# Optimization experiments

Measured on AMD Instinct MI355X. Metric: run time of the kernel, lower is better.

Reference implementation:

```python
import jax, jax.numpy as jnp
import numpy as np

B, T, D_IN, H, L4 = 64, 512, 512, 1024, 4096  # L4 = 4*H (torch LSTMCell gate dim)


def setup_inputs() -> dict:
    key = jax.random.key(0)
    ks = jax.random.split(key, 9)
    s_in = 1.0 / np.sqrt(H)  # torch LSTMCell default init scale
    return {
        "x": jax.random.normal(ks[0], (B, T, D_IN), dtype=jnp.float32),
        "Wih0": jax.random.normal(ks[1], (L4, D_IN), dtype=jnp.float32) * s_in,
        "Whh0": jax.random.normal(ks[2], (L4, H), dtype=jnp.float32) * s_in,
        "bih0": jax.random.normal(ks[3], (L4,), dtype=jnp.float32) * s_in,
        "bhh0": jax.random.normal(ks[4], (L4,), dtype=jnp.float32) * s_in,
        "Wih1": jax.random.normal(ks[5], (L4, H), dtype=jnp.float32) * s_in,
        "Whh1": jax.random.normal(ks[6], (L4, H), dtype=jnp.float32) * s_in,
        "bih1": jax.random.normal(ks[7], (L4,), dtype=jnp.float32) * s_in,
        "bhh1": jax.random.normal(ks[8], (L4,), dtype=jnp.float32) * s_in,
    }


def _lstm_cell(x, h, c, Wih, Whh, bih, bhh):
    # torch.nn.LSTMCell: gates ordered i, f, g, o
    gates = x @ Wih.T + bih + h @ Whh.T + bhh  # [B, 4H]
    i, f, g, o = jnp.split(gates, 4, axis=-1)
    i = jax.nn.sigmoid(i)
    f = jax.nn.sigmoid(f)
    g = jnp.tanh(g)
    o = jax.nn.sigmoid(o)
    c_new = f * c + i * g
    h_new = o * jnp.tanh(c_new)
    return h_new, c_new


def reference(x, Wih0, Whh0, bih0, bhh0, Wih1, Whh1, bih1, bhh1):
    b = x.shape[0]
    h0 = jnp.zeros((b, H), dtype=x.dtype)
    zeros4 = (h0, h0, h0, h0)  # (h0, c0, h1, c1)

    def step(carry, x_t):
        h0_, c0_, h1_, c1_ = carry
        h0_, c0_ = _lstm_cell(x_t, h0_, c0_, Wih0, Whh0, bih0, bhh0)
        h1_, c1_ = _lstm_cell(h0_, h1_, c1_, Wih1, Whh1, bih1, bhh1)
        return (h0_, c0_, h1_, c1_), h1_

    _, ys = jax.lax.scan(step, zeros4, jnp.swapaxes(x, 0, 1))  # ys: [T, B, H]
    return jax.nn.sigmoid(jnp.swapaxes(ys, 0, 1))  # [B, T, H]
```

## Files before the change

kernel.cpp:

```cpp
#include <hip/hip_runtime.h>
#include <hip/hip_bf16.h>

typedef __attribute__((ext_vector_type(8))) short short8;
typedef __attribute__((ext_vector_type(4))) float f32x4;
typedef __attribute__((ext_vector_type(4))) unsigned uint4v;
typedef unsigned long long u64;

#define T_STEPS 512
#define BATCH 64
#define HID 1024
#define DIN 512
#define NBLOCKS 128
#define NTHREADS 512

#define WS_GRP 0
#define WS_ROOT 2048
#define WS_H0 4096
#define WS_H1 (4096 + 262144)
#define WS_XB (1u << 20)
#define HBUF 131072

#define MFMA __builtin_amdgcn_mfma_f32_16x16x32_bf16

__device__ __forceinline__ short bf16r(float x) {
  unsigned u = __builtin_bit_cast(unsigned, x);
  u += 0x7FFFu + ((u >> 16) & 1u);
  return (short)(u >> 16);
}

__device__ __forceinline__ float sigf(float x) {
  return 1.0f / (1.0f + __expf(-x));
}
__device__ __forceinline__ float tanh_(float x) {
  return 2.0f * sigf(2.0f * x) - 1.0f;
}

__device__ __forceinline__ short8 pack8(const float* p) {
  float4 a = *(const float4*)p;
  float4 c = *(const float4*)(p + 4);
  short8 v;
  v[0] = bf16r(a.x); v[1] = bf16r(a.y); v[2] = bf16r(a.z); v[3] = bf16r(a.w);
  v[4] = bf16r(c.x); v[5] = bf16r(c.y); v[6] = bf16r(c.z); v[7] = bf16r(c.w);
  return v;
}

__device__ __forceinline__ short8 ld_frag16(const void* base, int voff) {
  __amdgpu_buffer_rsrc_t rsrc = __builtin_amdgcn_make_buffer_rsrc(
      const_cast<void*>(base), (short)0, 0xFFFFFFFFu, 0x00020000u);
  uint4v f = __builtin_amdgcn_raw_buffer_load_b128(rsrc, voff, 0, 0x11);
  return __builtin_bit_cast(short8, f);
}

__device__ __forceinline__ void wait_gen(unsigned* root, unsigned* gen_lds,
                                         unsigned s, int tid) {
  if (tid == 256) {
    const unsigned tgt = 8u * s;
    int g = 0;
    while (__hip_atomic_load(root, __ATOMIC_RELAXED, __HIP_MEMORY_SCOPE_AGENT) < tgt) {
      __builtin_amdgcn_s_sleep(2);
      if (++g > (1 << 13)) break;
    }
    __hip_atomic_store(gen_lds, s, __ATOMIC_RELEASE, __HIP_MEMORY_SCOPE_WORKGROUP);
  }
  int g = 0;
  while (__hip_atomic_load(gen_lds, __ATOMIC_ACQUIRE, __HIP_MEMORY_SCOPE_WORKGROUP) < s) {
    __builtin_amdgcn_s_sleep(1);
    if (++g > (1 << 17)) break;
  }
}

__global__ void cast_x_kernel(const float* __restrict__ x, unsigned char* __restrict__ ws) {
  unsigned char* xb = ws + WS_XB;
  int idx = blockIdx.x * blockDim.x + threadIdx.x;
  for (int c = idx; c < 64 * 512 * 64; c += 262144) {
    const int b = c >> 15;
    const int t = (c >> 6) & 511;
    const int kc = c & 63;
    const float* src = x + (((b << 9) + t) << 9) + (kc << 3);
    short8 v = pack8(src);
    const int kt = kc >> 2;
    const int ln = (b & 15) + ((kc & 3) << 4);
    unsigned char* dst = xb + (((t << 2) + (b >> 4)) * 16 + kt) * 1024 + ln * 16;
    *(short8*)dst = v;
  }
}

__global__ __launch_bounds__(NTHREADS, 1) void lstm_main(
    const float* __restrict__ Wih0, const float* __restrict__ Whh0,
    const float* __restrict__ bih0, const float* __restrict__ bhh0,
    const float* __restrict__ Wih1, const float* __restrict__ Whh1,
    const float* __restrict__ bih1, const float* __restrict__ bhh1,
    float* __restrict__ out, unsigned char* __restrict__ ws)
{
  __shared__ float red[8][4][2][64][4];
  __shared__ float red2[8][4][2][64][4];
  __shared__ unsigned gen_lds;

  const int tid = threadIdx.x;
  const int wid = tid >> 6;
  const int lane = tid & 63;
  const int blk = blockIdx.x;
  const int lane16 = lane * 16;

  unsigned* grp = (unsigned*)(ws + WS_GRP);
  unsigned* root = (unsigned*)(ws + WS_ROOT);
  unsigned char* h0b = ws + WS_H0;
  unsigned char* h1b = ws + WS_H1;
  const unsigned char* xb = ws + WS_XB;

  short8 wf[28];
  {
    const int hi8 = (lane >> 4) << 3;
#pragma unroll
    for (int nt = 0; nt < 2; ++nt) {
      const int n = nt * 16 + (lane & 15);
      const int row = ((n >> 3) << 10) + blk * 8 + (n & 7);
#pragma unroll
      for (int i = 0; i < 2; ++i)
        wf[i * 2 + nt] = pack8(Wih0 + row * DIN + (2 * wid + i) * 32 + hi8);
#pragma unroll
      for (int i = 0; i < 4; ++i) {
        const int k = (4 * wid + i) * 32 + hi8;
        wf[4 + i * 2 + nt]  = pack8(Whh0 + row * HID + k);
        wf[12 + i * 2 + nt] = pack8(Wih1 + row * HID + k);
        wf[20 + i * 2 + nt] = pack8(Whh1 + row * HID + k);
      }
    }
  }

  const int j = tid & 7;
  const int b = tid >> 3;
  const int jg = blk * 8 + j;
  const int m = b >> 4;
  const int r = b & 15;
  float bias0[4], bias1[4];
#pragma unroll
  for (int g = 0; g < 4; ++g) {
    bias0[g] = bih0[g * HID + jg] + bhh0[g * HID + jg];
    bias1[g] = bih1[g * HID + jg] + bhh1[g * HID + jg];
  }
  float c0 = 0.0f, c1 = 0.0f;
  const int hoff = ((b >> 4) * 32 + (jg >> 5)) * 1024 +
                   ((b & 15) + 16 * ((jg >> 3) & 3)) * 16 + (jg & 7) * 2;

  if (tid == 0) __hip_atomic_store(&gen_lds, 0u, __ATOMIC_RELAXED, __HIP_MEMORY_SCOPE_WORKGROUP);
  __syncthreads();

  for (int s = 0; s <= T_STEPS; ++s) {
    const int p0 = s & 1;
    const bool doL0 = (s < T_STEPS);
    const bool doL1 = (s >= 1);
    const unsigned char* h0r = h0b + (p0 ^ 1) * HBUF;
    const unsigned char* h1r = h1b + p0 * HBUF;

    f32x4 acc0[4][2];
    if (doL0) {
      const unsigned char* xs = xb + s * 65536;
#pragma unroll
      for (int mm = 0; mm < 4; ++mm) {
        acc0[mm][0] = (f32x4){0.f, 0.f, 0.f, 0.f};
        acc0[mm][1] = (f32x4){0.f, 0.f, 0.f, 0.f};
#pragma unroll
        for (int i = 0; i < 2; ++i) {
          short8 af = *(const short8*)(xs + (mm * 16 + 2 * wid + i) * 1024 + lane16);
          acc0[mm][0] = MFMA(af, wf[i * 2 + 0], acc0[mm][0], 0, 0, 0);
          acc0[mm][1] = MFMA(af, wf[i * 2 + 1], acc0[mm][1], 0, 0, 0);
        }
      }
    }

    wait_gen(root, &gen_lds, (unsigned)s, tid);

#pragma unroll
    for (int mm = 0; mm < 4; ++mm) {
      short8 f0[4], f1[4];
#pragma unroll
      for (int i = 0; i < 4; ++i)
        f0[i] = ld_frag16(h0r, (mm * 32 + 4 * wid + i) * 1024 + lane16);
      if (doL1) {
#pragma unroll
        for (int i = 0; i < 4; ++i)
          f1[i] = ld_frag16(h1r, (mm * 32 + 4 * wid + i) * 1024 + lane16);
      }

      if (doL0) {
#pragma unroll
        for (int i = 0; i < 4; ++i) {
          acc0[mm][0] = MFMA(f0[i], wf[4 + i * 2 + 0], acc0[mm][0], 0, 0, 0);
          acc0[mm][1] = MFMA(f0[i], wf[4 + i * 2 + 1], acc0[mm][1], 0, 0, 0);
        }
        *(f32x4*)(&red[wid][mm][0][lane][0]) = acc0[mm][0];
        *(f32x4*)(&red[wid][mm][1][lane][0]) = acc0[mm][1];
      }
      if (doL1) {
        f32x4 a1n0 = {0.f, 0.f, 0.f, 0.f}, a1n1 = {0.f, 0.f, 0.f, 0.f};
#pragma unroll
        for (int i = 0; i < 4; ++i) {
          a1n0 = MFMA(f0[i], wf[12 + i * 2 + 0], a1n0, 0, 0, 0);
          a1n1 = MFMA(f0[i], wf[12 + i * 2 + 1], a1n1, 0, 0, 0);
        }
#pragma unroll
        for (int i = 0; i < 4; ++i) {
          a1n0 = MFMA(f1[i], wf[20 + i * 2 + 0], a1n0, 0, 0, 0);
          a1n1 = MFMA(f1[i], wf[20 + i * 2 + 1], a1n1, 0, 0, 0);
        }
        *(f32x4*)(&red2[wid][mm][0][lane][0]) = a1n0;
        *(f32x4*)(&red2[wid][mm][1][lane][0]) = a1n1;
      }
    }
    __syncthreads();

    if (doL0) {
      float sg[4];
#pragma unroll
      for (int g = 0; g < 4; ++g) {
        const int n = g * 8 + j;
        const int nt = n >> 4;
        const int ln = ((r >> 2) << 4) | (n & 15);
        const int rg = r & 3;
        float t = bias0[g];
#pragma unroll
        for (int w2 = 0; w2 < 8; ++w2) t += red[w2][m][nt][ln][rg];
        sg[g] = t;
      }
      const float iv = sigf(sg[0]);
      const float fv = sigf(sg[1]);
      const float gv = tanh_(sg[2]);
      const float ov = sigf(sg[3]);
      c0 = fv * c0 + iv * gv;
      const float h0v = ov * tanh_(c0);
      unsigned hb = (unsigned)bf16r(h0v) & 0xFFFFu;
      unsigned nb = (unsigned)__shfl_down((int)hb, 1) & 0xFFFFu;
      if ((j & 1) == 0)
        __hip_atomic_store((unsigned*)(h0b + p0 * HBUF + hoff), hb | (nb << 16),
                           __ATOMIC_RELAXED, __HIP_MEMORY_SCOPE_AGENT);
    }
    float outv = 0.0f;
    if (doL1) {
      float sg[4];
#pragma unroll
      for (int g = 0; g < 4; ++g) {
        const int n = g * 8 + j;
        const int nt = n >> 4;
        const int ln = ((r >> 2) << 4) | (n & 15);
        const int rg = r & 3;
        float t = bias1[g];
#pragma unroll
        for (int w2 = 0; w2 < 8; ++w2) t += red2[w2][m][nt][ln][rg];
        sg[g] = t;
      }
      const float iv = sigf(sg[0]);
      const float fv = sigf(sg[1]);
      const float gv = tanh_(sg[2]);
      const float ov = sigf(sg[3]);
      c1 = fv * c1 + iv * gv;
      const float h1v = ov * tanh_(c1);
      outv = sigf(h1v);
      unsigned hb = (unsigned)bf16r(h1v) & 0xFFFFu;
      unsigned nb = (unsigned)__shfl_down((int)hb, 1) & 0xFFFFu;
      if ((j & 1) == 0)
        __hip_atomic_store((unsigned*)(h1b + (p0 ^ 1) * HBUF + hoff), hb | (nb << 16),
                           __ATOMIC_RELAXED, __HIP_MEMORY_SCOPE_AGENT);
    }

    asm volatile("s_waitcnt vmcnt(0)" ::: "memory");
    __syncthreads();

    if (doL0 && tid == 0) {
      unsigned v = __hip_atomic_fetch_add(&grp[(blk >> 4) * 32], 1u,
                                          __ATOMIC_RELAXED, __HIP_MEMORY_SCOPE_AGENT);
      if ((v & 15) == 15)
        __hip_atomic_fetch_add(root, 1u, __ATOMIC_RELAXED, __HIP_MEMORY_SCOPE_AGENT);
    }

    if (doL1)
      __builtin_nontemporal_store(outv, &out[b * (T_STEPS * HID) + (s - 1) * HID + jg]);
  }
}

extern "C" void kernel_launch(void* const* d_in, const int* in_sizes, int n_in,
                              void* d_out, int out_size, void* d_ws, size_t ws_size,
                              hipStream_t stream) {
  const float* x    = (const float*)d_in[0];
  const float* Wih0 = (const float*)d_in[1];
  const float* Whh0 = (const float*)d_in[2];
  const float* bih0 = (const float*)d_in[3];
  const float* bhh0 = (const float*)d_in[4];
  const float* Wih1 = (const float*)d_in[5];
  const float* Whh1 = (const float*)d_in[6];
  const float* bih1 = (const float*)d_in[7];
  const float* bhh1 = (const float*)d_in[8];
  unsigned char* ws = (unsigned char*)d_ws;

  (void)hipMemsetAsync(d_ws, 0, WS_XB, stream);
  hipLaunchKernelGGL(cast_x_kernel, dim3(1024), dim3(256), 0, stream, x, ws);
  hipLaunchKernelGGL(lstm_main, dim3(NBLOCKS), dim3(NTHREADS), 0, stream,
                     Wih0, Whh0, bih0, bhh0, Wih1, Whh1, bih1, bhh1,
                     (float*)d_out, ws);
}
```

Measured before the change: 3.301 ms.

## Split work across blocks by batch half and 16 hidden units

Changes the per-block work split from all 64 batch rows by 8 hidden units to 32 batch rows (mg) by 16 hidden units (ng). Each block keeps twice as many weight fragments in registers (56 short8 instead of 28) but reads only half of the h0/h1 state fragments from global memory each step. The intent is to halve the per-step global reads of recurrent state on the latency-bound critical path and to give each A fragment more MFMAs. The cost is much higher register pressure, which could cause spills.

```diff
diff --git a/kernel.cpp b/kernel.cpp
--- a/kernel.cpp
+++ b/kernel.cpp
@@ -92,14 +92,16 @@
     const float* __restrict__ bih1, const float* __restrict__ bhh1,
     float* __restrict__ out, unsigned char* __restrict__ ws)
 {
-  __shared__ float red[8][4][2][64][4];
-  __shared__ float red2[8][4][2][64][4];
+  __shared__ float red[8][2][4][64][4];
+  __shared__ float red2[8][2][4][64][4];
   __shared__ unsigned gen_lds;
 
   const int tid = threadIdx.x;
   const int wid = tid >> 6;
   const int lane = tid & 63;
   const int blk = blockIdx.x;
+  const int mg = blk >> 6;
+  const int ng = blk & 63;
   const int lane16 = lane * 16;
 
   unsigned* grp = (unsigned*)(ws + WS_GRP);
@@ -108,31 +110,31 @@
   unsigned char* h1b = ws + WS_H1;
   const unsigned char* xb = ws + WS_XB;
 
-  short8 wf[28];
+  short8 wf[56];
   {
     const int hi8 = (lane >> 4) << 3;
 #pragma unroll
-    for (int nt = 0; nt < 2; ++nt) {
-      const int n = nt * 16 + (lane & 15);
-      const int row = ((n >> 3) << 10) + blk * 8 + (n & 7);
-#pragma unroll
-      for (int i = 0; i < 2; ++i)
-        wf[i * 2 + nt] = pack8(Wih0 + row * DIN + (2 * wid + i) * 32 + hi8);
-#pragma unroll
-      for (int i = 0; i < 4; ++i) {
-        const int k = (4 * wid + i) * 32 + hi8;
-        wf[4 + i * 2 + nt]  = pack8(Whh0 + row * HID + k);
-        wf[12 + i * 2 + nt] = pack8(Wih1 + row * HID + k);
-        wf[20 + i * 2 + nt] = pack8(Whh1 + row * HID + k);
-      }
-    }
-  }
-
-  const int j = tid & 7;
-  const int b = tid >> 3;
-  const int jg = blk * 8 + j;
-  const int m = b >> 4;
-  const int r = b & 15;
+    for (int nt = 0; nt < 4; ++nt) {
+      const int row = (nt << 10) + ng * 16 + (lane & 15);
+#pragma unroll
+      for (int kt = 0; kt < 2; ++kt)
+        wf[kt * 4 + nt] = pack8(Wih0 + row * DIN + (2 * wid + kt) * 32 + hi8);
+#pragma unroll
+      for (int kt = 0; kt < 4; ++kt) {
+        const int k = (4 * wid + kt) * 32 + hi8;
+        wf[8 + kt * 4 + nt]  = pack8(Whh0 + row * HID + k);
+        wf[24 + kt * 4 + nt] = pack8(Wih1 + row * HID + k);
+        wf[40 + kt * 4 + nt] = pack8(Whh1 + row * HID + k);
+      }
+    }
+  }
+
+  const int j = tid & 15;
+  const int bl = tid >> 4;
+  const int b = mg * 32 + bl;
+  const int jg = ng * 16 + j;
+  const int m = bl >> 4;
+  const int r = bl & 15;
   float bias0[4], bias1[4];
 #pragma unroll
   for (int g = 0; g < 4; ++g) {
@@ -153,18 +155,20 @@
     const unsigned char* h0r = h0b + (p0 ^ 1) * HBUF;
     const unsigned char* h1r = h1b + p0 * HBUF;
 
-    f32x4 acc0[4][2];
+    f32x4 acc0[2][4];
     if (doL0) {
       const unsigned char* xs = xb + s * 65536;
 #pragma unroll
-      for (int mm = 0; mm < 4; ++mm) {
-        acc0[mm][0] = (f32x4){0.f, 0.f, 0.f, 0.f};
-        acc0[mm][1] = (f32x4){0.f, 0.f, 0.f, 0.f};
-#pragma unroll
-        for (int i = 0; i < 2; ++i) {
-          short8 af = *(const short8*)(xs + (mm * 16 + 2 * wid + i) * 1024 + lane16);
-          acc0[mm][0] = MFMA(af, wf[i * 2 + 0], acc0[mm][0], 0, 0, 0);
-          acc0[mm][1] = MFMA(af, wf[i * 2 + 1], acc0[mm][1], 0, 0, 0);
+      for (int mm = 0; mm < 2; ++mm) {
+#pragma unroll
+        for (int nt = 0; nt < 4; ++nt)
+          acc0[mm][nt] = (f32x4){0.f, 0.f, 0.f, 0.f};
+#pragma unroll
+        for (int kt = 0; kt < 2; ++kt) {
+          short8 af = *(const short8*)(xs + (((2 * mg + mm) * 16) + 2 * wid + kt) * 1024 + lane16);
+#pragma unroll
+          for (int nt = 0; nt < 4; ++nt)
+            acc0[mm][nt] = MFMA(af, wf[kt * 4 + nt], acc0[mm][nt], 0, 0, 0);
         }
       }
     }
@@ -172,40 +176,45 @@
     wait_gen(root, &gen_lds, (unsigned)s, tid);
 
 #pragma unroll
-    for (int mm = 0; mm < 4; ++mm) {
+    for (int mm = 0; mm < 2; ++mm) {
+      const int tbase = (2 * mg + mm) * 32 + 4 * wid;
       short8 f0[4], f1[4];
 #pragma unroll
       for (int i = 0; i < 4; ++i)
-        f0[i] = ld_frag16(h0r, (mm * 32 + 4 * wid + i) * 1024 + lane16);
+        f0[i] = ld_frag16(h0r, (tbase + i) * 1024 + lane16);
       if (doL1) {
 #pragma unroll
         for (int i = 0; i < 4; ++i)
-          f1[i] = ld_frag16(h1r, (mm * 32 + 4 * wid + i) * 1024 + lane16);
+          f1[i] = ld_frag16(h1r, (tbase + i) * 1024 + lane16);
       }
 
       if (doL0) {
 #pragma unroll
-        for (int i = 0; i < 4; ++i) {
-          acc0[mm][0] = MFMA(f0[i], wf[4 + i * 2 + 0], acc0[mm][0], 0, 0, 0);
-          acc0[mm][1] = MFMA(f0[i], wf[4 + i * 2 + 1], acc0[mm][1], 0, 0, 0);
-        }
-        *(f32x4*)(&red[wid][mm][0][lane][0]) = acc0[mm][0];
-        *(f32x4*)(&red[wid][mm][1][lane][0]) = acc0[mm][1];
+        for (int i = 0; i < 4; ++i)
+#pragma unroll
+          for (int nt = 0; nt < 4; ++nt)
+            acc0[mm][nt] = MFMA(f0[i], wf[8 + i * 4 + nt], acc0[mm][nt], 0, 0, 0);
+#pragma unroll
+        for (int nt = 0; nt < 4; ++nt)
+          *(f32x4*)(&red[wid][mm][nt][lane][0]) = acc0[mm][nt];
       }
       if (doL1) {
-        f32x4 a1n0 = {0.f, 0.f, 0.f, 0.f}, a1n1 = {0.f, 0.f, 0.f, 0.f};
-#pragma unroll
-        for (int i = 0; i < 4; ++i) {
-          a1n0 = MFMA(f0[i], wf[12 + i * 2 + 0], a1n0, 0, 0, 0);
-          a1n1 = MFMA(f0[i], wf[12 + i * 2 + 1], a1n1, 0, 0, 0);
-        }
-#pragma unroll
-        for (int i = 0; i < 4; ++i) {
-          a1n0 = MFMA(f1[i], wf[20 + i * 2 + 0], a1n0, 0, 0, 0);
-          a1n1 = MFMA(f1[i], wf[20 + i * 2 + 1], a1n1, 0, 0, 0);
-        }
-        *(f32x4*)(&red2[wid][mm][0][lane][0]) = a1n0;
-        *(f32x4*)(&red2[wid][mm][1][lane][0]) = a1n1;
+        f32x4 a1[4];
+#pragma unroll
+        for (int nt = 0; nt < 4; ++nt) a1[nt] = (f32x4){0.f, 0.f, 0.f, 0.f};
+#pragma unroll
+        for (int i = 0; i < 4; ++i)
+#pragma unroll
+          for (int nt = 0; nt < 4; ++nt)
+            a1[nt] = MFMA(f0[i], wf[24 + i * 4 + nt], a1[nt], 0, 0, 0);
+#pragma unroll
+        for (int i = 0; i < 4; ++i)
+#pragma unroll
+          for (int nt = 0; nt < 4; ++nt)
+            a1[nt] = MFMA(f1[i], wf[40 + i * 4 + nt], a1[nt], 0, 0, 0);
+#pragma unroll
+        for (int nt = 0; nt < 4; ++nt)
+          *(f32x4*)(&red2[wid][mm][nt][lane][0]) = a1[nt];
       }
     }
     __syncthreads();
@@ -214,13 +223,11 @@
       float sg[4];
 #pragma unroll
       for (int g = 0; g < 4; ++g) {
-        const int n = g * 8 + j;
-        const int nt = n >> 4;
-        const int ln = ((r >> 2) << 4) | (n & 15);
+        const int ln = ((r >> 2) << 4) | j;
         const int rg = r & 3;
         float t = bias0[g];
 #pragma unroll
-        for (int w2 = 0; w2 < 8; ++w2) t += red[w2][m][nt][ln][rg];
+        for (int w2 = 0; w2 < 8; ++w2) t += red[w2][m][g][ln][rg];
         sg[g] = t;
       }
       const float iv = sigf(sg[0]);
@@ -240,13 +247,11 @@
       float sg[4];
 #pragma unroll
       for (int g = 0; g < 4; ++g) {
-        const int n = g * 8 + j;
-        const int nt = n >> 4;
-        const int ln = ((r >> 2) << 4) | (n & 15);
+        const int ln = ((r >> 2) << 4) | j;
         const int rg = r & 3;
         float t = bias1[g];
 #pragma unroll
-        for (int w2 = 0; w2 < 8; ++w2) t += red2[w2][m][nt][ln][rg];
+        for (int w2 = 0; w2 < 8; ++w2) t += red2[w2][m][g][ln][rg];
         sg[g] = t;
       }
       const float iv = sigf(sg[0]);
```

After: 7.100 ms. 2.15x slower.

## Replace hierarchical root barrier with split per-layer group counters polled in parallel

Applied to the files above, without the earlier changes.

The two-level counter tree, where group counters feed a single root counter, is replaced by two sets of eight group counters, one for layer 0 and one for layer 1. A full wavefront polls all sixteen counters at once and combines the checks with a vote. Layer 0 now signals completion right after its h0 stores, before the layer-1 epilogue, so other blocks can start the next step sooner. The cost is an extra fence and __syncthreads per step, plus more polling traffic on global atomics.

```diff
diff --git a/kernel.cpp b/kernel.cpp
--- a/kernel.cpp
+++ b/kernel.cpp
@@ -13,8 +13,8 @@
 #define NBLOCKS 128
 #define NTHREADS 512
 
-#define WS_GRP 0
-#define WS_ROOT 2048
+#define WS_GRP0 0
+#define WS_GRP1 1024
 #define WS_H0 4096
 #define WS_H1 (4096 + 262144)
 #define WS_XB (1u << 20)
@@ -51,16 +51,22 @@
   return __builtin_bit_cast(short8, f);
 }
 
-__device__ __forceinline__ void wait_gen(unsigned* root, unsigned* gen_lds,
-                                         unsigned s, int tid) {
-  if (tid == 256) {
-    const unsigned tgt = 8u * s;
+__device__ __forceinline__ void wait_gen2(unsigned* grp0, unsigned* grp1,
+                                          unsigned* gen_lds, unsigned s, int tid) {
+  if ((tid >> 6) == 4) {
+    const int l = tid & 63;
+    const unsigned t0 = 16u * s;
+    const unsigned t1 = (s >= 1) ? 16u * (s - 1) : 0u;
     int g = 0;
-    while (__hip_atomic_load(root, __ATOMIC_RELAXED, __HIP_MEMORY_SCOPE_AGENT) < tgt) {
-      __builtin_amdgcn_s_sleep(2);
-      if (++g > (1 << 13)) break;
-    }
-    __hip_atomic_store(gen_lds, s, __ATOMIC_RELEASE, __HIP_MEMORY_SCOPE_WORKGROUP);
+    for (;;) {
+      unsigned v0 = (l < 8) ? __hip_atomic_load(&grp0[l * 32], __ATOMIC_RELAXED, __HIP_MEMORY_SCOPE_AGENT) : ~0u;
+      unsigned v1 = (l < 8) ? __hip_atomic_load(&grp1[l * 32], __ATOMIC_RELAXED, __HIP_MEMORY_SCOPE_AGENT) : ~0u;
+      if (__all(v0 >= t0 && v1 >= t1)) break;
+      __builtin_amdgcn_s_sleep(1);
+      if (++g > (1 << 15)) break;
+    }
+    if (l == 0)
+      __hip_atomic_store(gen_lds, s, __ATOMIC_RELEASE, __HIP_MEMORY_SCOPE_WORKGROUP);
   }
   int g = 0;
   while (__hip_atomic_load(gen_lds, __ATOMIC_ACQUIRE, __HIP_MEMORY_SCOPE_WORKGROUP) < s) {
@@ -102,8 +108,8 @@
   const int blk = blockIdx.x;
   const int lane16 = lane * 16;
 
-  unsigned* grp = (unsigned*)(ws + WS_GRP);
-  unsigned* root = (unsigned*)(ws + WS_ROOT);
+  unsigned* grp0 = (unsigned*)(ws + WS_GRP0);
+  unsigned* grp1 = (unsigned*)(ws + WS_GRP1);
   unsigned char* h0b = ws + WS_H0;
   unsigned char* h1b = ws + WS_H1;
   const unsigned char* xb = ws + WS_XB;
@@ -169,7 +175,7 @@
       }
     }
 
-    wait_gen(root, &gen_lds, (unsigned)s, tid);
+    wait_gen2(grp0, grp1, &gen_lds, (unsigned)s, tid);
 
 #pragma unroll
     for (int mm = 0; mm < 4; ++mm) {
@@ -235,6 +241,12 @@
         __hip_atomic_store((unsigned*)(h0b + p0 * HBUF + hoff), hb | (nb << 16),
                            __ATOMIC_RELAXED, __HIP_MEMORY_SCOPE_AGENT);
     }
+    asm volatile("s_waitcnt vmcnt(0)" ::: "memory");
+    __syncthreads();
+    if (doL0 && tid == 0)
+      __hip_atomic_fetch_add(&grp0[(blk >> 4) * 32], 1u,
+                             __ATOMIC_RELAXED, __HIP_MEMORY_SCOPE_AGENT);
+
     float outv = 0.0f;
     if (doL1) {
       float sg[4];
@@ -262,16 +274,11 @@
         __hip_atomic_store((unsigned*)(h1b + (p0 ^ 1) * HBUF + hoff), hb | (nb << 16),
                            __ATOMIC_RELAXED, __HIP_MEMORY_SCOPE_AGENT);
     }
-
     asm volatile("s_waitcnt vmcnt(0)" ::: "memory");
     __syncthreads();
-
-    if (doL0 && tid == 0) {
-      unsigned v = __hip_atomic_fetch_add(&grp[(blk >> 4) * 32], 1u,
-                                          __ATOMIC_RELAXED, __HIP_MEMORY_SCOPE_AGENT);
-      if ((v & 15) == 15)
-        __hip_atomic_fetch_add(root, 1u, __ATOMIC_RELAXED, __HIP_MEMORY_SCOPE_AGENT);
-    }
+    if (doL1 && tid == 0)
+      __hip_atomic_fetch_add(&grp1[(blk >> 4) * 32], 1u,
+                             __ATOMIC_RELAXED, __HIP_MEMORY_SCOPE_AGENT);
 
     if (doL1)
       __builtin_nontemporal_store(outv, &out[b * (T_STEPS * HID) + (s - 1) * HID + jg]);
```

After: 3.446 ms. 1.04x slower.
